# Kernel optimization log

Hardware: AMD Instinct MI355X
Metric: run time of the kernel (lower is better)

The kernel has to match this reference:

```python
import jax, jax.numpy as jnp
import numpy as np

EMBED_DIM = 256
NUM_HEADS = 8
HEAD_DIM = EMBED_DIM // NUM_HEADS
LN_EPS = 1e-5


def setup_inputs() -> dict:
    key = jax.random.key(0)
    ks = jax.random.split(key, 12)
    B, N_s, N_a, D = 4, 4096, 1024, EMBED_DIM
    xavier = lambda k: jax.random.uniform(k, (D, D), jnp.float32,
                                          -np.sqrt(6.0 / (2 * D)), np.sqrt(6.0 / (2 * D)))
    return {
        "satellite_tokens": jax.random.normal(ks[0], (B, N_s, D), jnp.float32),
        "auxiliary_tokens": jax.random.normal(ks[1], (B, N_a, D), jnp.float32),
        "Wq": xavier(ks[2]), "bq": jnp.zeros((D,), jnp.float32),
        "Wk": xavier(ks[3]), "bk": jnp.zeros((D,), jnp.float32),
        "Wv": xavier(ks[4]), "bv": jnp.zeros((D,), jnp.float32),
        "Wo": xavier(ks[5]), "bo": jnp.zeros((D,), jnp.float32),
        "ln_gamma": jnp.ones((D,), jnp.float32),
        "ln_beta": jnp.zeros((D,), jnp.float32),
    }


def _layernorm(x, gamma, beta):
    mu = jnp.mean(x, axis=-1, keepdims=True)
    var = jnp.var(x, axis=-1, keepdims=True)
    return (x - mu) * jax.lax.rsqrt(var + LN_EPS) * gamma + beta


def reference(satellite_tokens, auxiliary_tokens, Wq, bq, Wk, bk, Wv, bv, Wo, bo, ln_gamma, ln_beta):
    B, N_s, D = satellite_tokens.shape
    N_a = auxiliary_tokens.shape[1]
    H, hd = NUM_HEADS, HEAD_DIM
    scale = hd ** -0.5
    # Projections (torch Linear: x @ W.T + b)
    Q = (satellite_tokens @ Wq.T + bq).reshape(B, N_s, H, hd).transpose(0, 2, 1, 3)
    K = (auxiliary_tokens @ Wk.T + bk).reshape(B, N_a, H, hd).transpose(0, 2, 1, 3)
    V = (auxiliary_tokens @ Wv.T + bv).reshape(B, N_a, H, hd).transpose(0, 2, 1, 3)
    scores = jnp.einsum('bhsd,bhad->bhsa', Q, K) * scale  # (B,H,N_s,N_a)
    attn_weights = jax.nn.softmax(scores, axis=-1)
    # dropout is identity in eval mode
    attended = jnp.einsum('bhsa,bhad->bhsd', attn_weights, V)
    attended = attended.transpose(0, 2, 1, 3).reshape(B, N_s, D)
    attended = attended @ Wo.T + bo
    out = _layernorm(satellite_tokens + attended, ln_gamma, ln_beta)
    return out, attn_weights
```

## Files before the change

### kernel.cpp

```cpp
#include <hip/hip_runtime.h>

#define BATCH 4
#define NS 4096
#define NA 1024
#define DIM 256
#define NH 8
#define HD 32

typedef float f32x4 __attribute__((ext_vector_type(4)));
typedef __bf16 bf16x8 __attribute__((ext_vector_type(8)));
typedef __bf16 bf16x2 __attribute__((ext_vector_type(2)));
typedef unsigned short u16x8 __attribute__((ext_vector_type(8)));
typedef unsigned short u16x4 __attribute__((ext_vector_type(4)));
typedef unsigned int u32x4 __attribute__((ext_vector_type(4)));
typedef unsigned int u32x2 __attribute__((ext_vector_type(2)));
typedef unsigned int u32;

__device__ inline unsigned short f2bf(float f) {
  unsigned int u = __builtin_bit_cast(unsigned int, f);
  u = (u + 0x7FFFu + ((u >> 16) & 1u)) >> 16;
  return (unsigned short)u;
}

__device__ inline float bf2f(unsigned short u) {
  return __builtin_bit_cast(float, ((unsigned int)u) << 16);
}

__device__ inline f32x4 ld_f4(const float* p) {
  return *reinterpret_cast<const f32x4*>(p);
}

__device__ inline bf16x8 cvt_bf8(f32x4 a, f32x4 b) {
  u16x8 r;
  r[0] = f2bf(a[0]); r[1] = f2bf(a[1]); r[2] = f2bf(a[2]); r[3] = f2bf(a[3]);
  r[4] = f2bf(b[0]); r[5] = f2bf(b[1]); r[6] = f2bf(b[2]); r[7] = f2bf(b[3]);
  return __builtin_bit_cast(bf16x8, r);
}

__device__ inline bf16x8 ld_bf8(const unsigned short* p) {
  return __builtin_bit_cast(bf16x8, *reinterpret_cast<const u32x4*>(p));
}

__device__ inline f32x4 mfma16(bf16x8 a, bf16x8 b, f32x4 c) {
  return __builtin_amdgcn_mfma_f32_16x16x32_bf16(a, b, c, 0, 0, 0);
}

__device__ inline u32 pack_bf2(float lo, float hi) {
  bf16x2 t;
  t[0] = (__bf16)lo;
  t[1] = (__bf16)hi;
  return __builtin_bit_cast(u32, t);
}

__global__ __launch_bounds__(256)
void cast_weights(const float* __restrict__ Wq, const float* __restrict__ Wk,
                  const float* __restrict__ Wv, const float* __restrict__ Wo,
                  unsigned short* __restrict__ out)
{
  const int i = blockIdx.x * 256 + threadIdx.x;
  const int seg = i >> 14, off = (i & 16383) * 4;
  const float* src = seg == 0 ? Wq : seg == 1 ? Wk : seg == 2 ? Wv : Wo;
  f32x4 v = ld_f4(src + off);
  u16x4 r;
  r[0] = f2bf(v[0]); r[1] = f2bf(v[1]); r[2] = f2bf(v[2]); r[3] = f2bf(v[3]);
  *reinterpret_cast<u16x4*>(out + (size_t)seg * 65536 + off) = r;
}

__global__ __launch_bounds__(256)
void proj_qkv_fused(const float* __restrict__ sat, const float* __restrict__ aux,
                    const unsigned short* __restrict__ Wb,
                    const float* __restrict__ bq, const float* __restrict__ bk,
                    const float* __restrict__ bv,
                    unsigned short* __restrict__ Qb, unsigned short* __restrict__ Kb,
                    unsigned short* __restrict__ Vt)
{
  __shared__ unsigned short T[16][264];
  const int bid = blockIdx.x;
  const float* X; const unsigned short* W; const float* bias;
  unsigned short* out; int Ntok, r0, mode;
  if (bid < 1024)      { X = sat; W = Wb;          bias = bq; out = Qb; Ntok = NS; r0 = bid * 16;          mode = 0; }
  else if (bid < 1280) { X = aux; W = Wb + 65536;  bias = bk; out = Kb; Ntok = NA; r0 = (bid - 1024) * 16; mode = 0; }
  else                 { X = aux; W = Wb + 131072; bias = bv; out = Vt; Ntok = NA; r0 = (bid - 1280) * 16; mode = 1; }

  const int tid = threadIdx.x;
  const int wave = tid >> 6, lane = tid & 63, g = lane >> 4, c = lane & 15;
  const int nb = wave * 64;

  f32x4 acc[4] = {};
#pragma unroll
  for (int ks = 0; ks < 8; ++ks) {
    const int k0 = ks * 32 + g * 8;
    const float* xp = X + (size_t)(r0 + c) * DIM + k0;
    bf16x8 af = cvt_bf8(ld_f4(xp), ld_f4(xp + 4));
#pragma unroll
    for (int nt = 0; nt < 4; ++nt) {
      bf16x8 bf = ld_bf8(W + (size_t)(nb + nt * 16 + c) * DIM + k0);
      acc[nt] = mfma16(af, bf, acc[nt]);
    }
  }
#pragma unroll
  for (int nt = 0; nt < 4; ++nt)
#pragma unroll
    for (int i = 0; i < 4; ++i) {
      const int n = nb + nt * 16 + c;
      T[g * 4 + i][n] = f2bf(acc[nt][i] + bias[n]);
    }
  __syncthreads();

  const int b = r0 / Ntok;
  const int t0 = r0 % Ntok;
  if (mode == 0) {
    const int h = tid >> 5, rem = tid & 31;
    const int row = rem >> 1, d0 = (rem & 1) * 16;
    u32x4 lo = *reinterpret_cast<const u32x4*>(&T[row][h * 32 + d0]);
    u32x4 hi = *reinterpret_cast<const u32x4*>(&T[row][h * 32 + d0 + 8]);
    unsigned short* op = out + ((size_t)(b * NH + h) * Ntok + t0 + row) * HD + d0;
    *reinterpret_cast<u32x4*>(op) = lo;
    *reinterpret_cast<u32x4*>(op + 8) = hi;
  } else {
    const int h = tid >> 5, d = tid & 31;
    u16x8 w0, w1;
#pragma unroll
    for (int r = 0; r < 8; ++r) {
      w0[r] = T[r][tid];
      w1[r] = T[8 + r][tid];
    }
    unsigned short* op = out + ((size_t)(b * NH + h) * HD + d) * NA + t0;
    *reinterpret_cast<u16x8*>(op) = w0;
    *reinterpret_cast<u16x8*>(op + 8) = w1;
  }
}

__global__ __launch_bounds__(256, 4)
void attn_kernel(const unsigned short* __restrict__ Qb,
                 const unsigned short* __restrict__ Kb,
                 const unsigned short* __restrict__ Vt,
                 float* __restrict__ attn_out,
                 unsigned short* __restrict__ attw)
{
  __shared__ unsigned short P_lds[4][16][264];
  __shared__ u32 attp2[4][16][17];
  __shared__ float wred[4][16];

  const int blk = (blockIdx.x & 7) * 1024 + (blockIdx.x >> 3);
  const int bh = blk >> 8;
  const int s0 = (blk & 255) << 4;
  const int tid = threadIdx.x;
  const int wave = tid >> 6, lane = tid & 63, g = lane >> 4, c = lane & 15;
  const float expc = 0.17677669529663687f * 1.4426950408889634f;

  const unsigned short* Qp = Qb + ((size_t)bh * NS + s0) * HD;
  const unsigned short* Kp = Kb + (size_t)bh * NA * HD;
  const unsigned short* Vp = Vt + (size_t)bh * HD * NA;

  const bf16x8 qf = ld_bf8(Qp + (size_t)c * HD + g * 8);
  const int ab = wave * 256;

  f32x4 acc[16];
#pragma unroll
  for (int nt = 0; nt < 16; ++nt) {
    bf16x8 kf = ld_bf8(Kp + (size_t)(ab + nt * 16 + c) * HD + g * 8);
    f32x4 z = {0.f, 0.f, 0.f, 0.f};
    acc[nt] = mfma16(kf, qf, z);
  }

  float psum = 0.f;
#pragma unroll
  for (int nt = 0; nt < 16; ++nt)
#pragma unroll
    for (int i = 0; i < 4; ++i) {
      const float e = exp2f(acc[nt][i] * expc);
      acc[nt][i] = e;
      psum += e;
    }
  psum += __shfl_xor(psum, 16);
  psum += __shfl_xor(psum, 32);
  if (lane < 16) wred[wave][lane] = psum;
  __syncthreads();
  const float inv = 1.0f / (wred[0][c] + wred[1][c] + wred[2][c] + wred[3][c]);

#pragma unroll
  for (int nt = 0; nt < 16; ++nt) {
    f32x4 p = acc[nt] * inv;
    u32x2 pk;
    pk[0] = pack_bf2(p[0], p[1]);
    pk[1] = pack_bf2(p[2], p[3]);
    *reinterpret_cast<u32x2*>(&P_lds[wave][c][nt * 16 + g * 4]) = pk;
  }

  f32x4 o0 = {}, o1 = {};
#pragma unroll
  for (int ks = 0; ks < 8; ++ks) {
    const int kl = ks * 32 + g * 8;
    bf16x8 pf = ld_bf8(&P_lds[wave][c][kl]);
    bf16x8 v0 = ld_bf8(Vp + (size_t)c * NA + ab + kl);
    bf16x8 v1 = ld_bf8(Vp + (size_t)(16 + c) * NA + ab + kl);
    o0 = mfma16(pf, v0, o0);
    o1 = mfma16(pf, v1, o1);
  }
#pragma unroll
  for (int i = 0; i < 4; ++i)
    attp2[wave][g * 4 + i][c] = pack_bf2(o0[i], o1[i]);
  __syncthreads();

  const int b = bh >> 3, h = bh & 7;
#pragma unroll
  for (int t = tid; t < 512; t += 256) {
    const int row = t >> 5, col = t & 31;
    const int c2 = col & 15, hi = col >> 4;
    float s = 0.f;
#pragma unroll
    for (int w = 0; w < 4; ++w) {
      const u32 pk = attp2[w][row][c2];
      s += bf2f(hi ? (unsigned short)(pk >> 16) : (unsigned short)(pk & 0xffff));
    }
    attw[((size_t)b * NS + s0 + row) * DIM + h * HD + col] = f2bf(s);
  }

  float* aout = attn_out + ((size_t)bh * NS + s0) * NA;
#pragma unroll
  for (int rr = 0; rr < 4; ++rr) {
    const int row = wave * 4 + rr;
    float* rp = aout + (size_t)row * NA;
#pragma unroll
    for (int p = 0; p < 4; ++p) {
      u16x4 raw = *reinterpret_cast<const u16x4*>(&P_lds[p][row][lane * 4]);
      f32x4 o;
      o[0] = bf2f(raw[0]); o[1] = bf2f(raw[1]);
      o[2] = bf2f(raw[2]); o[3] = bf2f(raw[3]);
      *reinterpret_cast<f32x4*>(rp + p * 256 + lane * 4) = o;
    }
  }
}

__global__ __launch_bounds__(256)
void out_proj_ln(const unsigned short* __restrict__ attw,
                 const float* __restrict__ sat,
                 const unsigned short* __restrict__ Wob, const float* __restrict__ bo,
                 const float* __restrict__ gamma, const float* __restrict__ beta,
                 float* __restrict__ out)
{
  __shared__ float Y[16][DIM];
  const int r0 = blockIdx.x * 16;
  const int tid = threadIdx.x;
  const int wave = tid >> 6, lane = tid & 63, g = lane >> 4, c = lane & 15;
  const int nb = wave * 64;

  f32x4 acc[4] = {};
#pragma unroll
  for (int ks = 0; ks < 8; ++ks) {
    const int k0 = ks * 32 + g * 8;
    bf16x8 af = ld_bf8(attw + (size_t)(r0 + c) * DIM + k0);
#pragma unroll
    for (int nt = 0; nt < 4; ++nt) {
      bf16x8 bf = ld_bf8(Wob + (size_t)(nb + nt * 16 + c) * DIM + k0);
      acc[nt] = mfma16(af, bf, acc[nt]);
    }
  }
#pragma unroll
  for (int nt = 0; nt < 4; ++nt)
#pragma unroll
    for (int i = 0; i < 4; ++i) {
      const int row = g * 4 + i, n = nb + nt * 16 + c;
      Y[row][n] = acc[nt][i] + bo[n] + sat[(size_t)(r0 + row) * DIM + n];
    }
  __syncthreads();

  const int row = tid >> 4, tt = tid & 15;
  f32x4 v[4];
  float s = 0.f, ss = 0.f;
#pragma unroll
  for (int j = 0; j < 4; ++j) {
    v[j] = *reinterpret_cast<const f32x4*>(&Y[row][tt * 4 + 64 * j]);
#pragma unroll
    for (int e = 0; e < 4; ++e) { s += v[j][e]; ss += v[j][e] * v[j][e]; }
  }
#pragma unroll
  for (int off = 1; off < 16; off <<= 1) {
    s += __shfl_xor(s, off);
    ss += __shfl_xor(ss, off);
  }
  const float mu = s * (1.0f / 256.0f);
  const float var = ss * (1.0f / 256.0f) - mu * mu;
  const float rstd = rsqrtf(var + 1e-5f);
  float* op = out + (size_t)(r0 + row) * DIM;
#pragma unroll
  for (int j = 0; j < 4; ++j) {
    const int n0 = tt * 4 + 64 * j;
    f32x4 r;
#pragma unroll
    for (int e = 0; e < 4; ++e)
      r[e] = (v[j][e] - mu) * rstd * gamma[n0 + e] + beta[n0 + e];
    *reinterpret_cast<f32x4*>(op + n0) = r;
  }
}

extern "C" void kernel_launch(void* const* d_in, const int* in_sizes, int n_in,
                              void* d_out, int out_size, void* d_ws, size_t ws_size,
                              hipStream_t stream)
{
  (void)in_sizes; (void)n_in; (void)out_size; (void)ws_size;
  const float* sat   = (const float*)d_in[0];
  const float* aux   = (const float*)d_in[1];
  const float* Wq    = (const float*)d_in[2];
  const float* bq    = (const float*)d_in[3];
  const float* Wk    = (const float*)d_in[4];
  const float* bk    = (const float*)d_in[5];
  const float* Wv    = (const float*)d_in[6];
  const float* bv    = (const float*)d_in[7];
  const float* Wo    = (const float*)d_in[8];
  const float* bo    = (const float*)d_in[9];
  const float* gamma = (const float*)d_in[10];
  const float* beta  = (const float*)d_in[11];

  float* out = (float*)d_out;
  float* attn_out = out + (size_t)BATCH * NS * DIM;

  char* ws = (char*)d_ws;
  unsigned short* Qb   = (unsigned short*)(ws);
  unsigned short* Kb   = (unsigned short*)(ws + (8u << 20));
  unsigned short* Vt   = (unsigned short*)(ws + (10u << 20));
  unsigned short* attw = (unsigned short*)(ws + (12u << 20));
  unsigned short* Wb   = (unsigned short*)(ws + (20u << 20));
  unsigned short* Wob  = Wb + 3 * 65536;

  cast_weights<<<dim3(256), dim3(256), 0, stream>>>(Wq, Wk, Wv, Wo, Wb);
  proj_qkv_fused<<<dim3(1536), dim3(256), 0, stream>>>(sat, aux, Wb, bq, bk, bv, Qb, Kb, Vt);
  attn_kernel<<<dim3(8192), dim3(256), 0, stream>>>(Qb, Kb, Vt, attn_out, attw);
  out_proj_ln<<<dim3(BATCH * NS / 16), dim3(256), 0, stream>>>(attw, sat, Wob, bo, gamma, beta, out);
}
```

Baseline: 218.3 us.

## Make attention kernel persistent with K/V staged in LDS and shuffle-based P

The attention kernel now runs one block per (batch, head, 512-query chunk). Each block loads the whole K and V^T for its head into LDS once and loops over 32 query tiles, prefetching the next Q fragment. The probability tile is rearranged into MFMA A-operand layout with cross-lane shuffles instead of a round trip through LDS. The fp32 attention weights are stored straight from registers, which drops the bf16 rounding of the stored probabilities. The aim is to cut repeated global K/V reads and the LDS traffic for P. The cost is a grid of only 256 blocks with one block per CU (about 130 KB of LDS), so few waves are resident to hide latency. The large attention-weight stores are also split into 64-byte row segments instead of full contiguous rows.

```diff
diff --git a/kernel.cpp b/kernel.cpp
--- a/kernel.cpp
+++ b/kernel.cpp
@@ -13,7 +13,6 @@
 typedef unsigned short u16x8 __attribute__((ext_vector_type(8)));
 typedef unsigned short u16x4 __attribute__((ext_vector_type(4)));
 typedef unsigned int u32x4 __attribute__((ext_vector_type(4)));
-typedef unsigned int u32x2 __attribute__((ext_vector_type(2)));
 typedef unsigned int u32;
 
 __device__ inline unsigned short f2bf(float f) {
@@ -50,6 +49,11 @@
   t[0] = (__bf16)lo;
   t[1] = (__bf16)hi;
   return __builtin_bit_cast(u32, t);
+}
+
+__device__ inline void bar_lgkm() {
+  asm volatile("s_waitcnt lgkmcnt(0)" ::: "memory");
+  asm volatile("s_barrier" ::: "memory");
 }
 
 __global__ __launch_bounds__(256)
@@ -131,105 +135,139 @@
   }
 }
 
-__global__ __launch_bounds__(256, 4)
+__global__ __launch_bounds__(256, 1)
 void attn_kernel(const unsigned short* __restrict__ Qb,
                  const unsigned short* __restrict__ Kb,
                  const unsigned short* __restrict__ Vt,
                  float* __restrict__ attn_out,
                  unsigned short* __restrict__ attw)
 {
-  __shared__ unsigned short P_lds[4][16][264];
+  __shared__ unsigned short K_lds[1024 * 32];
+  __shared__ unsigned short V_lds[32][1032];
   __shared__ u32 attp2[4][16][17];
   __shared__ float wred[4][16];
 
-  const int blk = (blockIdx.x & 7) * 1024 + (blockIdx.x >> 3);
-  const int bh = blk >> 8;
-  const int s0 = (blk & 255) << 4;
+  const int blk = blockIdx.x;
+  const int bh = blk >> 3;
+  const int part = blk & 7;
   const int tid = threadIdx.x;
   const int wave = tid >> 6, lane = tid & 63, g = lane >> 4, c = lane & 15;
   const float expc = 0.17677669529663687f * 1.4426950408889634f;
 
-  const unsigned short* Qp = Qb + ((size_t)bh * NS + s0) * HD;
-  const unsigned short* Kp = Kb + (size_t)bh * NA * HD;
-  const unsigned short* Vp = Vt + (size_t)bh * HD * NA;
-
-  const bf16x8 qf = ld_bf8(Qp + (size_t)c * HD + g * 8);
+  const unsigned short* Kg = Kb + (size_t)bh * NA * HD;
+  const unsigned short* Vg = Vt + (size_t)bh * HD * NA;
+#pragma unroll
+  for (int i = 0; i < 16; ++i) {
+    const int idx = i * 256 + tid;
+    *reinterpret_cast<u32x4*>(&K_lds[idx * 8]) =
+        *reinterpret_cast<const u32x4*>(Kg + (size_t)idx * 8);
+  }
+#pragma unroll
+  for (int i = 0; i < 16; ++i) {
+    const int idx = i * 256 + tid;
+    const int r = idx >> 7, off = (idx & 127) * 8;
+    *reinterpret_cast<u32x4*>(&V_lds[r][off]) =
+        *reinterpret_cast<const u32x4*>(Vg + (size_t)r * NA + off);
+  }
+  __syncthreads();
+
   const int ab = wave * 256;
-
-  f32x4 acc[16];
-#pragma unroll
-  for (int nt = 0; nt < 16; ++nt) {
-    bf16x8 kf = ld_bf8(Kp + (size_t)(ab + nt * 16 + c) * HD + g * 8);
-    f32x4 z = {0.f, 0.f, 0.f, 0.f};
-    acc[nt] = mfma16(kf, qf, z);
-  }
-
-  float psum = 0.f;
-#pragma unroll
-  for (int nt = 0; nt < 16; ++nt)
-#pragma unroll
-    for (int i = 0; i < 4; ++i) {
-      const float e = exp2f(acc[nt][i] * expc);
-      acc[nt][i] = e;
-      psum += e;
-    }
-  psum += __shfl_xor(psum, 16);
-  psum += __shfl_xor(psum, 32);
-  if (lane < 16) wred[wave][lane] = psum;
-  __syncthreads();
-  const float inv = 1.0f / (wred[0][c] + wred[1][c] + wred[2][c] + wred[3][c]);
-
-#pragma unroll
-  for (int nt = 0; nt < 16; ++nt) {
-    f32x4 p = acc[nt] * inv;
-    u32x2 pk;
-    pk[0] = pack_bf2(p[0], p[1]);
-    pk[1] = pack_bf2(p[2], p[3]);
-    *reinterpret_cast<u32x2*>(&P_lds[wave][c][nt * 16 + g * 4]) = pk;
-  }
-
-  f32x4 o0 = {}, o1 = {};
-#pragma unroll
-  for (int ks = 0; ks < 8; ++ks) {
-    const int kl = ks * 32 + g * 8;
-    bf16x8 pf = ld_bf8(&P_lds[wave][c][kl]);
-    bf16x8 v0 = ld_bf8(Vp + (size_t)c * NA + ab + kl);
-    bf16x8 v1 = ld_bf8(Vp + (size_t)(16 + c) * NA + ab + kl);
-    o0 = mfma16(pf, v0, o0);
-    o1 = mfma16(pf, v1, o1);
-  }
-#pragma unroll
-  for (int i = 0; i < 4; ++i)
-    attp2[wave][g * 4 + i][c] = pack_bf2(o0[i], o1[i]);
-  __syncthreads();
-
   const int b = bh >> 3, h = bh & 7;
-#pragma unroll
-  for (int t = tid; t < 512; t += 256) {
-    const int row = t >> 5, col = t & 31;
-    const int c2 = col & 15, hi = col >> 4;
-    float s = 0.f;
-#pragma unroll
-    for (int w = 0; w < 4; ++w) {
-      const u32 pk = attp2[w][row][c2];
-      s += bf2f(hi ? (unsigned short)(pk >> 16) : (unsigned short)(pk & 0xffff));
-    }
-    attw[((size_t)b * NS + s0 + row) * DIM + h * HD + col] = f2bf(s);
-  }
-
-  float* aout = attn_out + ((size_t)bh * NS + s0) * NA;
-#pragma unroll
-  for (int rr = 0; rr < 4; ++rr) {
-    const int row = wave * 4 + rr;
-    float* rp = aout + (size_t)row * NA;
-#pragma unroll
-    for (int p = 0; p < 4; ++p) {
-      u16x4 raw = *reinterpret_cast<const u16x4*>(&P_lds[p][row][lane * 4]);
-      f32x4 o;
-      o[0] = bf2f(raw[0]); o[1] = bf2f(raw[1]);
-      o[2] = bf2f(raw[2]); o[3] = bf2f(raw[3]);
-      *reinterpret_cast<f32x4*>(rp + p * 256 + lane * 4) = o;
-    }
+  const int sA = ((lane >> 4) & 1) * 32 + c;
+  const int sB = sA + 16;
+  const bool hi = lane >= 32;
+
+  const unsigned short* Qp = Qb + ((size_t)bh * NS + part * 512) * HD;
+  bf16x8 qf = ld_bf8(Qp + (size_t)c * HD + g * 8);
+
+#pragma unroll 1
+  for (int it = 0; it < 32; ++it) {
+    const int s0 = part * 512 + it * 16;
+
+    bf16x8 qf_nxt = qf;
+    if (it < 31)
+      qf_nxt = ld_bf8(Qp + (size_t)((it + 1) * 16 + c) * HD + g * 8);
+
+    f32x4 acc[16];
+#pragma unroll
+    for (int nt = 0; nt < 16; ++nt) {
+      bf16x8 kf = ld_bf8(&K_lds[(ab + nt * 16 + c) * 32 + g * 8]);
+      f32x4 z = {0.f, 0.f, 0.f, 0.f};
+      acc[nt] = mfma16(kf, qf, z);
+    }
+
+    float psum = 0.f;
+#pragma unroll
+    for (int nt = 0; nt < 16; ++nt)
+#pragma unroll
+      for (int i = 0; i < 4; ++i) {
+        const float e = exp2f(acc[nt][i] * expc);
+        acc[nt][i] = e;
+        psum += e;
+      }
+    psum += __shfl_xor(psum, 16);
+    psum += __shfl_xor(psum, 32);
+    if (lane < 16) wred[wave][lane] = psum;
+    bar_lgkm();
+    const float inv = 1.0f / (wred[0][c] + wred[1][c] + wred[2][c] + wred[3][c]);
+
+#pragma unroll
+    for (int nt = 0; nt < 16; ++nt) acc[nt] *= inv;
+
+    u32 pkd[16][2];
+#pragma unroll
+    for (int nt = 0; nt < 16; ++nt) {
+      pkd[nt][0] = pack_bf2(acc[nt][0], acc[nt][1]);
+      pkd[nt][1] = pack_bf2(acc[nt][2], acc[nt][3]);
+    }
+
+    f32x4 o0 = {}, o1 = {};
+#pragma unroll
+    for (int ks = 0; ks < 8; ++ks) {
+      const int a0 = __shfl((int)pkd[2 * ks][0], sA);
+      const int a1 = __shfl((int)pkd[2 * ks][1], sA);
+      const int b0 = __shfl((int)pkd[2 * ks + 1][0], sA);
+      const int b1 = __shfl((int)pkd[2 * ks + 1][1], sA);
+      const int a2 = __shfl((int)pkd[2 * ks][0], sB);
+      const int a3 = __shfl((int)pkd[2 * ks][1], sB);
+      const int b2 = __shfl((int)pkd[2 * ks + 1][0], sB);
+      const int b3 = __shfl((int)pkd[2 * ks + 1][1], sB);
+      u32x4 paw;
+      paw[0] = (u32)(hi ? b0 : a0);
+      paw[1] = (u32)(hi ? b1 : a1);
+      paw[2] = (u32)(hi ? b2 : a2);
+      paw[3] = (u32)(hi ? b3 : a3);
+      const bf16x8 pa = __builtin_bit_cast(bf16x8, paw);
+      const int k0 = ab + ks * 32 + g * 8;
+      bf16x8 v0 = ld_bf8(&V_lds[c][k0]);
+      bf16x8 v1 = ld_bf8(&V_lds[16 + c][k0]);
+      o0 = mfma16(pa, v0, o0);
+      o1 = mfma16(pa, v1, o1);
+    }
+#pragma unroll
+    for (int i = 0; i < 4; ++i)
+      attp2[wave][g * 4 + i][c] = pack_bf2(o0[i], o1[i]);
+
+    float* aout = attn_out + ((size_t)bh * NS + s0) * NA;
+#pragma unroll
+    for (int nt = 0; nt < 16; ++nt)
+      *reinterpret_cast<f32x4*>(aout + (size_t)c * NA + ab + nt * 16 + g * 4) = acc[nt];
+
+    bar_lgkm();
+
+#pragma unroll
+    for (int t = tid; t < 512; t += 256) {
+      const int row = t >> 5, col = t & 31;
+      const int c2 = col & 15, hi2 = col >> 4;
+      float s = 0.f;
+#pragma unroll
+      for (int w = 0; w < 4; ++w) {
+        const u32 pk = attp2[w][row][c2];
+        s += bf2f(hi2 ? (unsigned short)(pk >> 16) : (unsigned short)(pk & 0xffff));
+      }
+      attw[((size_t)b * NS + s0 + row) * DIM + h * HD + col] = f2bf(s);
+    }
+    qf = qf_nxt;
   }
 }
 
@@ -326,6 +364,6 @@
 
   cast_weights<<<dim3(256), dim3(256), 0, stream>>>(Wq, Wk, Wv, Wo, Wb);
   proj_qkv_fused<<<dim3(1536), dim3(256), 0, stream>>>(sat, aux, Wb, bq, bk, bv, Qb, Kb, Vt);
-  attn_kernel<<<dim3(8192), dim3(256), 0, stream>>>(Qb, Kb, Vt, attn_out, attw);
+  attn_kernel<<<dim3(256), dim3(256), 0, stream>>>(Qb, Kb, Vt, attn_out, attw);
   out_proj_ln<<<dim3(BATCH * NS / 16), dim3(256), 0, stream>>>(attw, sat, Wob, bo, gamma, beta, out);
 }
```

After: 231.3 us. +6.0%, slower.

## Process 128 query rows per attention block, keeping K/V fragments in registers

Applied to the files above, without the earlier changes.

Each attention block now handles eight 16-row query tiles for one batch-head, loading the K and V fragments into registers once and reusing them across tiles instead of reloading per tile. P is double-buffered in LDS, and softmax normalization is deferred to the PV output and the attention-weight write, which removes a separate normalize pass. Barriers become raw s_waitcnt plus s_barrier. The grid shrinks to 1024 blocks with a lower occupancy hint. Register pressure rises and there is less parallelism to hide the dominant attn_out store traffic. The P fed into the PV product is now unnormalized bf16, which slightly changes rounding.

```diff
diff --git a/kernel.cpp b/kernel.cpp
--- a/kernel.cpp
+++ b/kernel.cpp
@@ -50,6 +50,11 @@
   t[0] = (__bf16)lo;
   t[1] = (__bf16)hi;
   return __builtin_bit_cast(u32, t);
+}
+
+__device__ inline void bar_lgkm() {
+  asm volatile("s_waitcnt lgkmcnt(0)" ::: "memory");
+  asm volatile("s_barrier" ::: "memory");
 }
 
 __global__ __launch_bounds__(256)
@@ -131,104 +136,115 @@
   }
 }
 
-__global__ __launch_bounds__(256, 4)
+__global__ __launch_bounds__(256, 2)
 void attn_kernel(const unsigned short* __restrict__ Qb,
                  const unsigned short* __restrict__ Kb,
                  const unsigned short* __restrict__ Vt,
                  float* __restrict__ attn_out,
                  unsigned short* __restrict__ attw)
 {
-  __shared__ unsigned short P_lds[4][16][264];
+  __shared__ unsigned short P_lds[2][4][16][264];
   __shared__ u32 attp2[4][16][17];
-  __shared__ float wred[4][16];
-
-  const int blk = (blockIdx.x & 7) * 1024 + (blockIdx.x >> 3);
-  const int bh = blk >> 8;
-  const int s0 = (blk & 255) << 4;
+  __shared__ float wred[2][4][16];
+
+  const int bid = blockIdx.x;
+  const int blk = (bid & 7) * 128 + (bid >> 3);
+  const int bh = blk >> 5;
+  const int row0 = (blk & 31) << 7;
   const int tid = threadIdx.x;
   const int wave = tid >> 6, lane = tid & 63, g = lane >> 4, c = lane & 15;
   const float expc = 0.17677669529663687f * 1.4426950408889634f;
 
-  const unsigned short* Qp = Qb + ((size_t)bh * NS + s0) * HD;
-  const unsigned short* Kp = Kb + (size_t)bh * NA * HD;
-  const unsigned short* Vp = Vt + (size_t)bh * HD * NA;
-
-  const bf16x8 qf = ld_bf8(Qp + (size_t)c * HD + g * 8);
+  const unsigned short* Kg = Kb + (size_t)bh * NA * HD;
+  const unsigned short* Vg = Vt + (size_t)bh * HD * NA;
+  const unsigned short* Qp = Qb + ((size_t)bh * NS + row0) * HD;
   const int ab = wave * 256;
-
-  f32x4 acc[16];
-#pragma unroll
-  for (int nt = 0; nt < 16; ++nt) {
-    bf16x8 kf = ld_bf8(Kp + (size_t)(ab + nt * 16 + c) * HD + g * 8);
-    f32x4 z = {0.f, 0.f, 0.f, 0.f};
-    acc[nt] = mfma16(kf, qf, z);
-  }
-
-  float psum = 0.f;
+  const int b = bh >> 3, h = bh & 7;
+
+  bf16x8 kfr[16], v0r[8], v1r[8], qfr[8];
 #pragma unroll
   for (int nt = 0; nt < 16; ++nt)
+    kfr[nt] = ld_bf8(Kg + (size_t)(ab + nt * 16 + c) * HD + g * 8);
+#pragma unroll
+  for (int ks = 0; ks < 8; ++ks) {
+    v0r[ks] = ld_bf8(Vg + (size_t)c * NA + ab + ks * 32 + g * 8);
+    v1r[ks] = ld_bf8(Vg + (size_t)(16 + c) * NA + ab + ks * 32 + g * 8);
+  }
+#pragma unroll
+  for (int t = 0; t < 8; ++t)
+    qfr[t] = ld_bf8(Qp + (size_t)(t * 16 + c) * HD + g * 8);
+
+#pragma unroll
+  for (int it = 0; it < 8; ++it) {
+    const int pb = it & 1;
+    const int s0 = row0 + it * 16;
+
+    float psum = 0.f;
+#pragma unroll
+    for (int nt = 0; nt < 16; ++nt) {
+      f32x4 z = {0.f, 0.f, 0.f, 0.f};
+      f32x4 a = mfma16(kfr[nt], qfr[it], z);
+      float e0 = exp2f(a[0] * expc), e1 = exp2f(a[1] * expc);
+      float e2 = exp2f(a[2] * expc), e3 = exp2f(a[3] * expc);
+      psum += (e0 + e1) + (e2 + e3);
+      u32x2 pk;
+      pk[0] = pack_bf2(e0, e1);
+      pk[1] = pack_bf2(e2, e3);
+      *reinterpret_cast<u32x2*>(&P_lds[pb][wave][c][nt * 16 + g * 4]) = pk;
+    }
+    psum += __shfl_xor(psum, 16);
+    psum += __shfl_xor(psum, 32);
+    if (lane < 16) wred[pb][wave][lane] = psum;
+    bar_lgkm();
+
+    float invo[4];
 #pragma unroll
     for (int i = 0; i < 4; ++i) {
-      const float e = exp2f(acc[nt][i] * expc);
-      acc[nt][i] = e;
-      psum += e;
-    }
-  psum += __shfl_xor(psum, 16);
-  psum += __shfl_xor(psum, 32);
-  if (lane < 16) wred[wave][lane] = psum;
-  __syncthreads();
-  const float inv = 1.0f / (wred[0][c] + wred[1][c] + wred[2][c] + wred[3][c]);
-
-#pragma unroll
-  for (int nt = 0; nt < 16; ++nt) {
-    f32x4 p = acc[nt] * inv;
-    u32x2 pk;
-    pk[0] = pack_bf2(p[0], p[1]);
-    pk[1] = pack_bf2(p[2], p[3]);
-    *reinterpret_cast<u32x2*>(&P_lds[wave][c][nt * 16 + g * 4]) = pk;
-  }
-
-  f32x4 o0 = {}, o1 = {};
-#pragma unroll
-  for (int ks = 0; ks < 8; ++ks) {
-    const int kl = ks * 32 + g * 8;
-    bf16x8 pf = ld_bf8(&P_lds[wave][c][kl]);
-    bf16x8 v0 = ld_bf8(Vp + (size_t)c * NA + ab + kl);
-    bf16x8 v1 = ld_bf8(Vp + (size_t)(16 + c) * NA + ab + kl);
-    o0 = mfma16(pf, v0, o0);
-    o1 = mfma16(pf, v1, o1);
-  }
-#pragma unroll
-  for (int i = 0; i < 4; ++i)
-    attp2[wave][g * 4 + i][c] = pack_bf2(o0[i], o1[i]);
-  __syncthreads();
-
-  const int b = bh >> 3, h = bh & 7;
-#pragma unroll
-  for (int t = tid; t < 512; t += 256) {
-    const int row = t >> 5, col = t & 31;
-    const int c2 = col & 15, hi = col >> 4;
-    float s = 0.f;
-#pragma unroll
-    for (int w = 0; w < 4; ++w) {
-      const u32 pk = attp2[w][row][c2];
-      s += bf2f(hi ? (unsigned short)(pk >> 16) : (unsigned short)(pk & 0xffff));
-    }
-    attw[((size_t)b * NS + s0 + row) * DIM + h * HD + col] = f2bf(s);
-  }
-
-  float* aout = attn_out + ((size_t)bh * NS + s0) * NA;
-#pragma unroll
-  for (int rr = 0; rr < 4; ++rr) {
-    const int row = wave * 4 + rr;
-    float* rp = aout + (size_t)row * NA;
-#pragma unroll
-    for (int p = 0; p < 4; ++p) {
-      u16x4 raw = *reinterpret_cast<const u16x4*>(&P_lds[p][row][lane * 4]);
-      f32x4 o;
-      o[0] = bf2f(raw[0]); o[1] = bf2f(raw[1]);
-      o[2] = bf2f(raw[2]); o[3] = bf2f(raw[3]);
-      *reinterpret_cast<f32x4*>(rp + p * 256 + lane * 4) = o;
+      const int r = g * 4 + i;
+      invo[i] = 1.0f / (wred[pb][0][r] + wred[pb][1][r] +
+                        wred[pb][2][r] + wred[pb][3][r]);
+    }
+
+    f32x4 o0 = {}, o1 = {};
+#pragma unroll
+    for (int ks = 0; ks < 8; ++ks) {
+      bf16x8 pf = ld_bf8(&P_lds[pb][wave][c][ks * 32 + g * 8]);
+      o0 = mfma16(pf, v0r[ks], o0);
+      o1 = mfma16(pf, v1r[ks], o1);
+    }
+#pragma unroll
+    for (int i = 0; i < 4; ++i)
+      attp2[wave][g * 4 + i][c] = pack_bf2(o0[i] * invo[i], o1[i] * invo[i]);
+    bar_lgkm();
+
+#pragma unroll
+    for (int t = tid; t < 512; t += 256) {
+      const int row = t >> 5, col = t & 31;
+      const int c2 = col & 15, hi2 = col >> 4;
+      float s = 0.f;
+#pragma unroll
+      for (int w = 0; w < 4; ++w) {
+        const u32 pk = attp2[w][row][c2];
+        s += bf2f(hi2 ? (unsigned short)(pk >> 16) : (unsigned short)(pk & 0xffff));
+      }
+      attw[((size_t)b * NS + s0 + row) * DIM + h * HD + col] = f2bf(s);
+    }
+
+    float* aout = attn_out + ((size_t)bh * NS + s0) * NA;
+#pragma unroll
+    for (int rr = 0; rr < 4; ++rr) {
+      const int row = wave * 4 + rr;
+      const float invr = 1.0f / (wred[pb][0][row] + wred[pb][1][row] +
+                                 wred[pb][2][row] + wred[pb][3][row]);
+      float* rp = aout + (size_t)row * NA;
+#pragma unroll
+      for (int p = 0; p < 4; ++p) {
+        u16x4 raw = *reinterpret_cast<const u16x4*>(&P_lds[pb][p][row][lane * 4]);
+        f32x4 o;
+        o[0] = bf2f(raw[0]) * invr; o[1] = bf2f(raw[1]) * invr;
+        o[2] = bf2f(raw[2]) * invr; o[3] = bf2f(raw[3]) * invr;
+        *reinterpret_cast<f32x4*>(rp + p * 256 + lane * 4) = o;
+      }
     }
   }
 }
@@ -326,6 +342,6 @@
 
   cast_weights<<<dim3(256), dim3(256), 0, stream>>>(Wq, Wk, Wv, Wo, Wb);
   proj_qkv_fused<<<dim3(1536), dim3(256), 0, stream>>>(sat, aux, Wb, bq, bk, bv, Qb, Kb, Vt);
-  attn_kernel<<<dim3(8192), dim3(256), 0, stream>>>(Qb, Kb, Vt, attn_out, attw);
+  attn_kernel<<<dim3(1024), dim3(256), 0, stream>>>(Qb, Kb, Vt, attn_out, attw);
   out_proj_ln<<<dim3(BATCH * NS / 16), dim3(256), 0, stream>>>(attw, sat, Wob, bo, gamma, beta, out);
 }
```

After: 194.5 us. 10.9% less time.
